# Performance work log

Measured on AMD Instinct MI355X. Metric: run time of the kernel, lower is better.

The kernel has to match this reference:

```python
import jax, jax.numpy as jnp
import numpy as np

NUM_HEADS = 8
T = 8  # hardcoded temporal dim in the original forward
MD = 3  # max_displacement -> 7x7 window
EPS = 1e-12  # F.normalize eps


def l2_normalize(x, axis):
    n = jnp.sqrt(jnp.sum(x * x, axis=axis, keepdims=True))
    return x / jnp.maximum(n, EPS)


def correlation_7x7(q, k):
    # q, k: [B, C, H, W]; FlowNet-style correlation, kernel_size=1, max_disp=3.
    # out[b, u, v, h, w] = sum_c q[b,c,h,w] * k[b,c,h+u-3,w+v-3] (zero padded)
    B, C, H, W = q.shape
    kp = jnp.pad(k, ((0, 0), (0, 0), (MD, MD), (MD, MD)))
    outs = []
    for dy in range(2 * MD + 1):
        for dx in range(2 * MD + 1):
            ks = kp[:, :, dy:dy + H, dx:dx + W]
            outs.append(jnp.sum(q * ks, axis=1))  # [B, H, W]
    corr = jnp.stack(outs, axis=1)  # [B, 49, H, W]
    return corr.reshape(B, 2 * MD + 1, 2 * MD + 1, H, W)


def setup_inputs() -> dict:
    key = jax.random.key(0)
    ks = jax.random.split(key, 6)
    B, N, C = 8, 8192, 256
    hd = C // NUM_HEADS
    std = 0.02
    return {
        "x": jax.random.normal(ks[0], (B, N, C), dtype=jnp.float32),
        "w_qk": jax.random.normal(ks[1], (2 * C, C), dtype=jnp.float32) * std,
        "w_corr": jax.random.normal(ks[2], (hd, 49), dtype=jnp.float32) * std,
        "b_corr": jnp.zeros((hd,), dtype=jnp.float32),
        "w_proj": jax.random.normal(ks[3], (C, C), dtype=jnp.float32) * std,
        "b_proj": jnp.zeros((C,), dtype=jnp.float32),
    }


def reference(x, w_qk, w_corr, b_corr, w_proj, b_proj):
    B, N, C = x.shape
    nh = NUM_HEADS
    hd = C // nh
    H = int(np.sqrt(N // T))
    W = H

    # qk projection (no bias): [B, N, 2C] -> q, k each [B, nh, N, hd]
    qk = jnp.einsum('bnc,dc->bnd', x, w_qk)
    qk = qk.reshape(B, N, 2, nh, hd).transpose(2, 0, 3, 1, 4)
    q, k = qk[0], qk[1]

    # 'b n (t h w) d -> (b n) t d h w'
    q = q.reshape(B * nh, T, H, W, hd).transpose(0, 1, 4, 2, 3)
    k = k.reshape(B * nh, T, H, W, hd).transpose(0, 1, 4, 2, 3)

    # temporal postfix: k[t+1], last frame repeated
    k_post = jnp.concatenate([k[:, 1:], k[:, -1:]], axis=1)

    qp = q.reshape(B * nh * T, hd, H, W)
    kp = k_post.reshape(B * nh * T, hd, H, W)
    qp = l2_normalize(qp, axis=1)
    kp = l2_normalize(kp, axis=1)

    corr = correlation_7x7(qp, kp)  # [(B nh T), 7, 7, H, W]
    # 'b u v h w -> b (h w) (u v)'
    corr = corr.transpose(0, 3, 4, 1, 2).reshape(B * nh * T, H * W, 49)

    v = jnp.einsum('bpk,dk->bpd', corr, w_corr) + b_corr  # [(B nh T), HW, hd]

    # '(b n t) (h w) d -> b n (t h w) d' then 'b h n d -> b n (h d)'
    out = v.reshape(B, nh, T * H * W, hd).transpose(0, 2, 1, 3).reshape(B, N, C)
    out = jnp.einsum('bnc,dc->bnd', out, w_proj) + b_proj
    return out
```

## Files before the change

### kernel.cpp

```cpp
#include <hip/hip_runtime.h>

typedef _Float16 half8 __attribute__((ext_vector_type(8)));
typedef _Float16 half2v __attribute__((ext_vector_type(2)));
typedef float float4v __attribute__((ext_vector_type(4)));

__device__ __forceinline__ float dot2acc(unsigned a, unsigned b, float c) {
#if __has_builtin(__builtin_amdgcn_fdot2)
  return __builtin_amdgcn_fdot2(__builtin_bit_cast(half2v, a), __builtin_bit_cast(half2v, b), c, false);
#else
  half2v ha = __builtin_bit_cast(half2v, a);
  half2v hb = __builtin_bit_cast(half2v, b);
  c += (float)ha[0] * (float)hb[0];
  c += (float)ha[1] * (float)hb[1];
  return c;
#endif
}
__device__ __forceinline__ unsigned hscale(unsigned a, float s) {
  half2v ha = __builtin_bit_cast(half2v, a);
  half2v r;
  r[0] = (_Float16)((float)ha[0] * s);
  r[1] = (_Float16)((float)ha[1] * s);
  return __builtin_bit_cast(unsigned, r);
}
__device__ __forceinline__ void gload_lds16(const void* g, void* l) {
  __builtin_amdgcn_global_load_lds((const __attribute__((address_space(1))) unsigned*)g,
                                   (__attribute__((address_space(3))) unsigned*)l, 16, 0, 0);
}

__global__ void cvt_all(const float4* __restrict__ x, const float4* __restrict__ wqk,
                        const float4* __restrict__ wpj,
                        ushort4* __restrict__ x16, ushort4* __restrict__ wqk16,
                        ushort4* __restrict__ wpj16) {
  int b = blockIdx.x;
  const float4* s;
  ushort4* d;
  int i;
  if (b < 16384) { s = x; d = x16; i = b * 256 + threadIdx.x; }
  else if (b < 16512) { s = wqk; d = wqk16; i = (b - 16384) * 256 + threadIdx.x; }
  else { s = wpj; d = wpj16; i = (b - 16512) * 256 + threadIdx.x; }
  float4 v = s[i];
  _Float16 a = (_Float16)v.x, bb = (_Float16)v.y, c = (_Float16)v.z, e = (_Float16)v.w;
  ushort4 o;
  o.x = __builtin_bit_cast(unsigned short, a);
  o.y = __builtin_bit_cast(unsigned short, bb);
  o.z = __builtin_bit_cast(unsigned short, c);
  o.w = __builtin_bit_cast(unsigned short, e);
  d[i] = o;
}

__global__ __launch_bounds__(256, 2)
void gemm_qk(const _Float16* __restrict__ A, const _Float16* __restrict__ Bw,
             _Float16* __restrict__ qo, _Float16* __restrict__ ko) {
  __shared__ _Float16 Ash[4096];
  __shared__ _Float16 Bsh[4096];
  const int tid = threadIdx.x;
  const int lane = tid & 63, w = tid >> 6;
  const int wm = w >> 1, wn = w & 1;
  const int ml = lane & 15, qd = lane >> 4;
  const int m0 = blockIdx.y * 128, n0 = blockIdx.x * 128;

  float4v acc[4][4];
  float4v z = {0.f, 0.f, 0.f, 0.f};
#pragma unroll
  for (int i = 0; i < 4; ++i)
#pragma unroll
    for (int j = 0; j < 4; ++j) acc[i][j] = z;

  const _Float16* Ap = A + (size_t)m0 * 256;
  const _Float16* Bp = Bw + (size_t)n0 * 256;
  const int gr = w * 64 + lane;
  const int row0 = gr >> 2, kb = gr & 3;

  for (int kt = 0; kt < 8; ++kt) {
    int k0 = kt * 32;
    gload_lds16(Ap + row0 * 256 + k0 + kb * 8, Ash + (size_t)(w * 64) * 8);
    gload_lds16(Ap + (row0 + 64) * 256 + k0 + kb * 8, Ash + (size_t)(256 + w * 64) * 8);
    gload_lds16(Bp + row0 * 256 + k0 + kb * 8, Bsh + (size_t)(w * 64) * 8);
    gload_lds16(Bp + (row0 + 64) * 256 + k0 + kb * 8, Bsh + (size_t)(256 + w * 64) * 8);
    __syncthreads();
    half8 af[4], bf[4];
#pragma unroll
    for (int im = 0; im < 4; ++im) {
      af[im] = *(const half8*)(Ash + (wm * 64 + im * 16 + ml) * 32 + qd * 8);
      bf[im] = *(const half8*)(Bsh + (wn * 64 + im * 16 + ml) * 32 + qd * 8);
    }
#pragma unroll
    for (int im = 0; im < 4; ++im)
#pragma unroll
      for (int in = 0; in < 4; ++in)
        acc[im][in] = __builtin_amdgcn_mfma_f32_16x16x32_f16(af[im], bf[in], acc[im][in], 0, 0, 0);
    __syncthreads();
  }

#pragma unroll
  for (int im = 0; im < 4; ++im) {
    int rowr0 = m0 + wm * 64 + im * 16 + qd * 4;
#pragma unroll
    for (int in = 0; in < 4; ++in) {
      int col = n0 + wn * 64 + in * 16 + ml;
      int s = col >> 8, h = (col >> 5) & 7, j = col & 31;
      _Float16* dst = s ? ko : qo;
#pragma unroll
      for (int r = 0; r < 4; ++r) {
        int rowr = rowr0 + r;
        int b = rowr >> 13, n = rowr & 8191;
        int t = n >> 10, yx = n & 1023;
        int p = b * 64 + h * 8 + t;
        dst[((size_t)p * 1024 + yx) * 32 + j] = (_Float16)acc[im][in][r];
      }
    }
  }
}

__global__ __launch_bounds__(256, 4)
void corr_kernel(const _Float16* __restrict__ q16, const _Float16* __restrict__ k16,
                 const float* __restrict__ wcorr, const float* __restrict__ bcorr,
                 _Float16* __restrict__ outp) {
  __shared__ uint4 smem[2304];
  __shared__ uint4 wcs[256];

  const int tid = threadIdx.x;
  const int bx = blockIdx.x;
  const int p = bx >> 2, tile = bx & 3;
  const int y0 = (tile >> 1) * 16, x0 = (tile & 1) * 16;
  const int b = p >> 6, h = (p >> 3) & 7, t = p & 7;
  const int pk = (t < 7) ? p + 1 : p;
  const int ty = tid >> 4, tx = tid & 15;

  _Float16* wch = (_Float16*)wcs;
  for (int idx = tid; idx < 2048; idx += 256) {
    int d = idx >> 6, kk = idx & 63;
    float v = (kk < 49) ? wcorr[d * 49 + kk] : (kk == 49 ? bcorr[d] : 0.f);
    wch[idx] = (_Float16)v;
  }

  const _Float16* kbase = k16 + (size_t)pk * 32768;
#pragma unroll
  for (int i = 0; i < 8; ++i) {
    int g = tid + i * 256;
    if (g < 1936) {
      int vec = g >> 2, part = g & 3;
      int ky = vec / 22, kx = vec - ky * 22;
      int gy = y0 + ky - 3, gx = x0 + kx - 3;
      uint4 val = make_uint4(0u, 0u, 0u, 0u);
      if (gy >= 0 && gy < 32 && gx >= 0 && gx < 32)
        val = *(const uint4*)(kbase + ((size_t)gy * 32 + gx) * 32 + part * 8);
      int slot = (vec << 2) | (part ^ (vec & 3) ^ ((vec >> 2) & 3));
      smem[slot] = val;
    }
  }
  __syncthreads();

  for (int v = tid; v < 484; v += 256) {
    int base = v << 2;
    int sw = (v & 3) ^ ((v >> 2) & 3);
    uint4 gg[4];
#pragma unroll
    for (int pq = 0; pq < 4; ++pq) gg[pq] = smem[base | (pq ^ sw)];
    float ss = 0.f;
#pragma unroll
    for (int pq = 0; pq < 4; ++pq) {
      const unsigned* u = (const unsigned*)&gg[pq];
#pragma unroll
      for (int e = 0; e < 4; ++e) ss = dot2acc(u[e], u[e], ss);
    }
    float sc = 1.f / fmaxf(sqrtf(ss), 1e-12f);
#pragma unroll
    for (int pq = 0; pq < 4; ++pq) {
      unsigned* u = (unsigned*)&gg[pq];
#pragma unroll
      for (int e = 0; e < 4; ++e) u[e] = hscale(u[e], sc);
      smem[base | (pq ^ sw)] = gg[pq];
    }
  }
  __syncthreads();

  const _Float16* qptr = q16 + (size_t)p * 32768 + ((size_t)(y0 + ty) * 32 + (x0 + tx)) * 32;
  uint4 qv[4];
#pragma unroll
  for (int i = 0; i < 4; ++i) qv[i] = *(const uint4*)(qptr + i * 8);
  unsigned* qu = (unsigned*)qv;
  float qss = 0.f;
#pragma unroll
  for (int e = 0; e < 16; ++e) qss = dot2acc(qu[e], qu[e], qss);
  float qsc = 1.f / fmaxf(sqrtf(qss), 1e-12f);
#pragma unroll
  for (int e = 0; e < 16; ++e) qu[e] = hscale(qu[e], qsc);

  float corr[49];
#pragma unroll
  for (int dy = 0; dy < 7; ++dy) {
#pragma unroll
    for (int dx = 0; dx < 7; ++dx) {
      int vec = (ty + dy) * 22 + (tx + dx);
      int base = vec << 2;
      int sw = (vec & 3) ^ ((vec >> 2) & 3);
      float c = 0.f;
#pragma unroll
      for (int pq = 0; pq < 4; ++pq) {
        uint4 kk = smem[base | (pq ^ sw)];
        const unsigned* ku = (const unsigned*)&kk;
#pragma unroll
        for (int e = 0; e < 4; ++e) c = dot2acc(qu[pq * 4 + e], ku[e], c);
      }
      corr[dy * 7 + dx] = c;
    }
  }
  __syncthreads();

#pragma unroll
  for (int i = 0; i < 8; ++i) {
    uint4 val;
    unsigned* vu = (unsigned*)&val;
#pragma unroll
    for (int e = 0; e < 4; ++e) {
      int idx = i * 8 + e * 2;
      half2v hh;
      hh[0] = (_Float16)(idx < 49 ? corr[idx] : (idx == 49 ? 1.f : 0.f));
      hh[1] = (_Float16)(idx + 1 < 49 ? corr[idx + 1] : (idx + 1 == 49 ? 1.f : 0.f));
      vu[e] = __builtin_bit_cast(unsigned, hh);
    }
    smem[tid * 9 + i] = val;
  }
  __syncthreads();

  _Float16* corrm = (_Float16*)smem;
  const int lane = tid & 63, w = tid >> 6;
  const int ml = lane & 15, qd = lane >> 4;
  float4v vacc[4][2];
  float4v z = {0.f, 0.f, 0.f, 0.f};
#pragma unroll
  for (int im = 0; im < 4; ++im) { vacc[im][0] = z; vacc[im][1] = z; }
#pragma unroll
  for (int ks = 0; ks < 2; ++ks) {
    half8 bfrag[2];
#pragma unroll
    for (int nt = 0; nt < 2; ++nt)
      bfrag[nt] = *(const half8*)(wch + (nt * 16 + ml) * 64 + ks * 32 + qd * 8);
#pragma unroll
    for (int im = 0; im < 4; ++im) {
      half8 afrag = *(const half8*)(corrm + (w * 64 + im * 16 + ml) * 72 + ks * 32 + qd * 8);
#pragma unroll
      for (int nt = 0; nt < 2; ++nt)
        vacc[im][nt] = __builtin_amdgcn_mfma_f32_16x16x32_f16(afrag, bfrag[nt], vacc[im][nt], 0, 0, 0);
    }
  }

#pragma unroll
  for (int im = 0; im < 4; ++im) {
#pragma unroll
    for (int nt = 0; nt < 2; ++nt) {
      int d = nt * 16 + ml;
#pragma unroll
      for (int r = 0; r < 4; ++r) {
        int pos = w * 64 + im * 16 + qd * 4 + r;
        int py = pos >> 4, px = pos & 15;
        int n = t * 1024 + (y0 + py) * 32 + (x0 + px);
        outp[(((size_t)b * 8192 + n) << 8) + h * 32 + d] = (_Float16)vacc[im][nt][r];
      }
    }
  }
}

__global__ __launch_bounds__(256, 2)
void gemm_proj(const _Float16* __restrict__ A, const _Float16* __restrict__ Bw,
               const float* __restrict__ bp, float* __restrict__ out) {
  __shared__ _Float16 Ash[4096];
  __shared__ _Float16 Bsh[4096];
  const int tid = threadIdx.x;
  const int lane = tid & 63, w = tid >> 6;
  const int wm = w >> 1, wn = w & 1;
  const int ml = lane & 15, qd = lane >> 4;
  const int m0 = blockIdx.y * 128, n0 = blockIdx.x * 128;

  float4v acc[4][4];
  float4v z = {0.f, 0.f, 0.f, 0.f};
#pragma unroll
  for (int i = 0; i < 4; ++i)
#pragma unroll
    for (int j = 0; j < 4; ++j) acc[i][j] = z;

  const _Float16* Ap = A + (size_t)m0 * 256;
  const _Float16* Bp = Bw + (size_t)n0 * 256;
  const int gr = w * 64 + lane;
  const int row0 = gr >> 2, kb = gr & 3;

  for (int kt = 0; kt < 8; ++kt) {
    int k0 = kt * 32;
    gload_lds16(Ap + row0 * 256 + k0 + kb * 8, Ash + (size_t)(w * 64) * 8);
    gload_lds16(Ap + (row0 + 64) * 256 + k0 + kb * 8, Ash + (size_t)(256 + w * 64) * 8);
    gload_lds16(Bp + row0 * 256 + k0 + kb * 8, Bsh + (size_t)(w * 64) * 8);
    gload_lds16(Bp + (row0 + 64) * 256 + k0 + kb * 8, Bsh + (size_t)(256 + w * 64) * 8);
    __syncthreads();
    half8 af[4], bf[4];
#pragma unroll
    for (int im = 0; im < 4; ++im) {
      af[im] = *(const half8*)(Ash + (wm * 64 + im * 16 + ml) * 32 + qd * 8);
      bf[im] = *(const half8*)(Bsh + (wn * 64 + im * 16 + ml) * 32 + qd * 8);
    }
#pragma unroll
    for (int im = 0; im < 4; ++im)
#pragma unroll
      for (int in = 0; in < 4; ++in)
        acc[im][in] = __builtin_amdgcn_mfma_f32_16x16x32_f16(af[im], bf[in], acc[im][in], 0, 0, 0);
    __syncthreads();
  }

#pragma unroll
  for (int im = 0; im < 4; ++im) {
    int rowr0 = m0 + wm * 64 + im * 16 + qd * 4;
#pragma unroll
    for (int in = 0; in < 4; ++in) {
      int col = n0 + wn * 64 + in * 16 + ml;
      float bias = bp[col];
#pragma unroll
      for (int r = 0; r < 4; ++r)
        out[(size_t)(rowr0 + r) * 256 + col] = acc[im][in][r] + bias;
    }
  }
}

extern "C" void kernel_launch(void* const* d_in, const int* in_sizes, int n_in,
                              void* d_out, int out_size, void* d_ws, size_t ws_size,
                              hipStream_t stream) {
  const float* x      = (const float*)d_in[0];
  const float* w_qk   = (const float*)d_in[1];
  const float* w_corr = (const float*)d_in[2];
  const float* b_corr = (const float*)d_in[3];
  const float* w_proj = (const float*)d_in[4];
  const float* b_proj = (const float*)d_in[5];
  float* out = (float*)d_out;

  char* ws = (char*)d_ws;
  _Float16* x16   = (_Float16*)(ws);
  _Float16* q16   = (_Float16*)(ws + 33554432);
  _Float16* k16   = (_Float16*)(ws + 67108864);
  _Float16* op16  = (_Float16*)(ws + 100663296);
  _Float16* wqk16 = (_Float16*)(ws + 134217728);
  _Float16* wpj16 = (_Float16*)(ws + 134479872);

  cvt_all<<<16576, 256, 0, stream>>>((const float4*)x, (const float4*)w_qk, (const float4*)w_proj,
                                     (ushort4*)x16, (ushort4*)wqk16, (ushort4*)wpj16);
  gemm_qk<<<dim3(4, 512), 256, 0, stream>>>(x16, wqk16, q16, k16);
  corr_kernel<<<2048, 256, 0, stream>>>(q16, k16, w_corr, b_corr, op16);
  gemm_proj<<<dim3(2, 512), 256, 0, stream>>>(op16, wpj16, b_proj, out);
}
```

Measured before the change: 235.0 us.

## Swap MFMA operands for vectorized epilogue stores and use a planar LDS layout in corr

```diff
diff --git a/kernel.cpp b/kernel.cpp
--- a/kernel.cpp
+++ b/kernel.cpp
@@ -25,6 +25,10 @@
 __device__ __forceinline__ void gload_lds16(const void* g, void* l) {
   __builtin_amdgcn_global_load_lds((const __attribute__((address_space(1))) unsigned*)g,
                                    (__attribute__((address_space(3))) unsigned*)l, 16, 0, 0);
+}
+__device__ __forceinline__ unsigned short h2u(float v) {
+  _Float16 h = (_Float16)v;
+  return __builtin_bit_cast(unsigned short, h);
 }
 
 __global__ void cvt_all(const float4* __restrict__ x, const float4* __restrict__ wqk,
@@ -39,12 +43,8 @@
   else if (b < 16512) { s = wqk; d = wqk16; i = (b - 16384) * 256 + threadIdx.x; }
   else { s = wpj; d = wpj16; i = (b - 16512) * 256 + threadIdx.x; }
   float4 v = s[i];
-  _Float16 a = (_Float16)v.x, bb = (_Float16)v.y, c = (_Float16)v.z, e = (_Float16)v.w;
   ushort4 o;
-  o.x = __builtin_bit_cast(unsigned short, a);
-  o.y = __builtin_bit_cast(unsigned short, bb);
-  o.z = __builtin_bit_cast(unsigned short, c);
-  o.w = __builtin_bit_cast(unsigned short, e);
+  o.x = h2u(v.x); o.y = h2u(v.y); o.z = h2u(v.z); o.w = h2u(v.w);
   d[i] = o;
 }
 
@@ -88,26 +88,27 @@
     for (int im = 0; im < 4; ++im)
 #pragma unroll
       for (int in = 0; in < 4; ++in)
-        acc[im][in] = __builtin_amdgcn_mfma_f32_16x16x32_f16(af[im], bf[in], acc[im][in], 0, 0, 0);
+        acc[im][in] = __builtin_amdgcn_mfma_f32_16x16x32_f16(bf[in], af[im], acc[im][in], 0, 0, 0);
     __syncthreads();
   }
 
 #pragma unroll
   for (int im = 0; im < 4; ++im) {
-    int rowr0 = m0 + wm * 64 + im * 16 + qd * 4;
+    int rowr = m0 + wm * 64 + im * 16 + ml;
+    int b = rowr >> 13, nn = rowr & 8191;
+    int t = nn >> 10, yx = nn & 1023;
 #pragma unroll
     for (int in = 0; in < 4; ++in) {
-      int col = n0 + wn * 64 + in * 16 + ml;
-      int s = col >> 8, h = (col >> 5) & 7, j = col & 31;
+      int nc0 = n0 + wn * 64 + in * 16 + qd * 4;
+      int s = nc0 >> 8, h = (nc0 >> 5) & 7, j0 = nc0 & 31;
       _Float16* dst = s ? ko : qo;
-#pragma unroll
-      for (int r = 0; r < 4; ++r) {
-        int rowr = rowr0 + r;
-        int b = rowr >> 13, n = rowr & 8191;
-        int t = n >> 10, yx = n & 1023;
-        int p = b * 64 + h * 8 + t;
-        dst[((size_t)p * 1024 + yx) * 32 + j] = (_Float16)acc[im][in][r];
-      }
+      ushort4 pk;
+      pk.x = h2u(acc[im][in][0]);
+      pk.y = h2u(acc[im][in][1]);
+      pk.z = h2u(acc[im][in][2]);
+      pk.w = h2u(acc[im][in][3]);
+      int p = b * 64 + h * 8 + t;
+      *(ushort4*)(dst + ((size_t)p * 1024 + yx) * 32 + j0) = pk;
     }
   }
 }
@@ -145,18 +146,15 @@
       uint4 val = make_uint4(0u, 0u, 0u, 0u);
       if (gy >= 0 && gy < 32 && gx >= 0 && gx < 32)
         val = *(const uint4*)(kbase + ((size_t)gy * 32 + gx) * 32 + part * 8);
-      int slot = (vec << 2) | (part ^ (vec & 3) ^ ((vec >> 2) & 3));
-      smem[slot] = val;
+      smem[part * 485 + vec] = val;
     }
   }
   __syncthreads();
 
   for (int v = tid; v < 484; v += 256) {
-    int base = v << 2;
-    int sw = (v & 3) ^ ((v >> 2) & 3);
     uint4 gg[4];
 #pragma unroll
-    for (int pq = 0; pq < 4; ++pq) gg[pq] = smem[base | (pq ^ sw)];
+    for (int pq = 0; pq < 4; ++pq) gg[pq] = smem[pq * 485 + v];
     float ss = 0.f;
 #pragma unroll
     for (int pq = 0; pq < 4; ++pq) {
@@ -170,7 +168,7 @@
       unsigned* u = (unsigned*)&gg[pq];
 #pragma unroll
       for (int e = 0; e < 4; ++e) u[e] = hscale(u[e], sc);
-      smem[base | (pq ^ sw)] = gg[pq];
+      smem[pq * 485 + v] = gg[pq];
     }
   }
   __syncthreads();
@@ -187,23 +185,25 @@
 #pragma unroll
   for (int e = 0; e < 16; ++e) qu[e] = hscale(qu[e], qsc);
 
+  const uint4* kwin = smem + (ty * 22 + tx);
   float corr[49];
 #pragma unroll
-  for (int dy = 0; dy < 7; ++dy) {
-#pragma unroll
-    for (int dx = 0; dx < 7; ++dx) {
-      int vec = (ty + dy) * 22 + (tx + dx);
-      int base = vec << 2;
-      int sw = (vec & 3) ^ ((vec >> 2) & 3);
-      float c = 0.f;
-#pragma unroll
-      for (int pq = 0; pq < 4; ++pq) {
-        uint4 kk = smem[base | (pq ^ sw)];
+  for (int i = 0; i < 49; ++i) corr[i] = 0.f;
+#pragma unroll
+  for (int pq = 0; pq < 4; ++pq) {
+#pragma unroll
+    for (int dy = 0; dy < 7; ++dy) {
+#pragma unroll
+      for (int dx = 0; dx < 7; ++dx) {
+        uint4 kk = kwin[pq * 485 + dy * 22 + dx];
         const unsigned* ku = (const unsigned*)&kk;
-#pragma unroll
-        for (int e = 0; e < 4; ++e) c = dot2acc(qu[pq * 4 + e], ku[e], c);
+        float c = corr[dy * 7 + dx];
+        c = dot2acc(qu[pq * 4 + 0], ku[0], c);
+        c = dot2acc(qu[pq * 4 + 1], ku[1], c);
+        c = dot2acc(qu[pq * 4 + 2], ku[2], c);
+        c = dot2acc(qu[pq * 4 + 3], ku[3], c);
+        corr[dy * 7 + dx] = c;
       }
-      corr[dy * 7 + dx] = c;
     }
   }
   __syncthreads();
@@ -242,22 +242,24 @@
       half8 afrag = *(const half8*)(corrm + (w * 64 + im * 16 + ml) * 72 + ks * 32 + qd * 8);
 #pragma unroll
       for (int nt = 0; nt < 2; ++nt)
-        vacc[im][nt] = __builtin_amdgcn_mfma_f32_16x16x32_f16(afrag, bfrag[nt], vacc[im][nt], 0, 0, 0);
+        vacc[im][nt] = __builtin_amdgcn_mfma_f32_16x16x32_f16(bfrag[nt], afrag, vacc[im][nt], 0, 0, 0);
     }
   }
 
 #pragma unroll
   for (int im = 0; im < 4; ++im) {
+    int pos = w * 64 + im * 16 + ml;
+    int py = pos >> 4, px = pos & 15;
+    int n = t * 1024 + (y0 + py) * 32 + (x0 + px);
 #pragma unroll
     for (int nt = 0; nt < 2; ++nt) {
-      int d = nt * 16 + ml;
-#pragma unroll
-      for (int r = 0; r < 4; ++r) {
-        int pos = w * 64 + im * 16 + qd * 4 + r;
-        int py = pos >> 4, px = pos & 15;
-        int n = t * 1024 + (y0 + py) * 32 + (x0 + px);
-        outp[(((size_t)b * 8192 + n) << 8) + h * 32 + d] = (_Float16)vacc[im][nt][r];
-      }
+      int d0 = nt * 16 + qd * 4;
+      ushort4 pkv;
+      pkv.x = h2u(vacc[im][nt][0]);
+      pkv.y = h2u(vacc[im][nt][1]);
+      pkv.z = h2u(vacc[im][nt][2]);
+      pkv.w = h2u(vacc[im][nt][3]);
+      *(ushort4*)(outp + (((size_t)b * 8192 + n) << 8) + h * 32 + d0) = pkv;
     }
   }
 }
@@ -302,20 +304,23 @@
     for (int im = 0; im < 4; ++im)
 #pragma unroll
       for (int in = 0; in < 4; ++in)
-        acc[im][in] = __builtin_amdgcn_mfma_f32_16x16x32_f16(af[im], bf[in], acc[im][in], 0, 0, 0);
+        acc[im][in] = __builtin_amdgcn_mfma_f32_16x16x32_f16(bf[in], af[im], acc[im][in], 0, 0, 0);
     __syncthreads();
   }
 
 #pragma unroll
   for (int im = 0; im < 4; ++im) {
-    int rowr0 = m0 + wm * 64 + im * 16 + qd * 4;
+    int rowr = m0 + wm * 64 + im * 16 + ml;
 #pragma unroll
     for (int in = 0; in < 4; ++in) {
-      int col = n0 + wn * 64 + in * 16 + ml;
-      float bias = bp[col];
-#pragma unroll
-      for (int r = 0; r < 4; ++r)
-        out[(size_t)(rowr0 + r) * 256 + col] = acc[im][in][r] + bias;
+      int nc0 = n0 + wn * 64 + in * 16 + qd * 4;
+      float4 bias = *(const float4*)(bp + nc0);
+      float4 v;
+      v.x = acc[im][in][0] + bias.x;
+      v.y = acc[im][in][1] + bias.y;
+      v.z = acc[im][in][2] + bias.z;
+      v.w = acc[im][in][3] + bias.w;
+      *(float4*)(out + (size_t)rowr * 256 + nc0) = v;
     }
   }
 }
```

Measured after the change: 235.2 us. Within noise of the previous version (+0.1%).
